# Performance work log

Hardware: AMD Instinct MI355X
Metric: run time of the kernel (lower is better)

The kernel has to match this reference:

```python
import jax, jax.numpy as jnp
import numpy as np

N = 1048576
N_GRID = 256
DX = 1.0 / N_GRID
INV_DX = float(N_GRID)
DT = 2e-5
P_VOL = (DX * 0.5) ** 2
P_RHO = 1.0
P_MASS = P_VOL * P_RHO
E_MOD = 1000.0
NU = 0.2
MU_0 = E_MOD / (2.0 * (1.0 + NU))
LAM_0 = E_MOD * NU / ((1.0 + NU) * (1.0 - 2.0 * NU))
GRAVITY = 50.0


def setup_inputs() -> dict:
    key = jax.random.key(0)
    k = jax.random.split(key, 5)
    x = 0.1 + 0.8 * jax.random.uniform(k[0], (N, 2), dtype=jnp.float32)
    v = 0.1 * jax.random.normal(k[1], (N, 2), dtype=jnp.float32)
    C = 0.5 * jax.random.normal(k[2], (N, 2, 2), dtype=jnp.float32)
    F = jnp.eye(2, dtype=jnp.float32)[None] + 0.1 * jax.random.normal(k[3], (N, 2, 2), dtype=jnp.float32)
    material = jax.random.randint(k[4], (N,), 0, 3, dtype=jnp.int32)
    Jp = jnp.ones((N,), dtype=jnp.float32)
    return {"x": x, "v": v, "C": C, "F": F, "material": material, "Jp": Jp}


def reference(x, v, C, F, material, Jp):
    dt, inv_dx, dx = DT, INV_DX, DX
    base = jnp.floor(x * inv_dx - 0.5).astype(jnp.int32)          # [N,2]
    fx = x * inv_dx - base.astype(x.dtype)                        # [N,2]
    # quadratic B-spline weights, stacked over the 3 taps -> [3,N,2]
    w = jnp.stack([0.5 * (1.5 - fx) ** 2,
                   0.75 - (fx - 1.0) ** 2,
                   0.5 * (fx - 0.5) ** 2], axis=0)

    # deformation gradient update
    F = F + dt * jnp.einsum('nij,njk->nik', C, F)

    h = jnp.exp(10.0 * (1.0 - Jp))
    h = jnp.where(material == 1, 0.3, h)
    mu = jnp.where(material == 0, 0.0, MU_0 * h)
    lam = LAM_0 * h

    # per-particle 2x2 SVD (original pads to 3x3 and slices back)
    U, sig, Vh = jnp.linalg.svd(F)

    # snow plasticity: clamp singular values, track Jp
    clamped = jnp.clip(sig, 1.0 - 2.5e-2, 1.0 + 4.5e-3)
    is_snow = material == 2
    Jp = jnp.where(is_snow, Jp * jnp.prod(sig / clamped, axis=-1), Jp)
    sig = jnp.where(is_snow[:, None], clamped, sig)

    J = jnp.prod(sig, axis=-1)
    eye2 = jnp.eye(2, dtype=x.dtype)
    F_fluid = eye2[None] * jnp.sqrt(J)[:, None, None]             # J^(1/n_dim), n_dim=2
    F_snow = jnp.einsum('nij,nj,njk->nik', U, sig, Vh)
    F = jnp.where((material == 0)[:, None, None], F_fluid,
                  jnp.where(is_snow[:, None, None], F_snow, F))

    R = jnp.einsum('nij,njk->nik', U, Vh)
    stress = (2.0 * mu[:, None, None] * jnp.einsum('nij,nkj->nik', F - R, F)
              + eye2[None] * (lam * J * (J - 1.0))[:, None, None])
    stress = (-dt * P_VOL * 4.0 * inv_dx ** 2) * stress
    affine = stress + P_MASS * C                                   # [N,2,2]

    # ---- P2G scatter over the 3x3 stencil (vectorized over 9 taps) ----
    offs = jnp.array([[i, j] for i in range(3) for j in range(3)], dtype=jnp.int32)  # [9,2]
    weight = w[offs[:, 0], :, 0] * w[offs[:, 1], :, 1]             # [9,N]
    target = base[None, :, :] + offs[:, None, :]                   # [9,N,2]
    idx = target[..., 0] * N_GRID + target[..., 1]                 # [9,N]
    flat_idx = idx.reshape(-1)
    NG2 = N_GRID * N_GRID

    v_add = P_MASS * v - jnp.einsum('nij,nj->ni', affine, x)       # [N,2]
    grid_v = jax.ops.segment_sum((weight[..., None] * v_add[None]).reshape(-1, 2),
                                 flat_idx, num_segments=NG2).reshape(N_GRID, N_GRID, 2)
    grid_affine = jax.ops.segment_sum((weight[..., None, None] * affine[None]).reshape(-1, 4),
                                      flat_idx, num_segments=NG2).reshape(N_GRID, N_GRID, 2, 2)
    grid_m = jax.ops.segment_sum((weight * P_MASS).reshape(-1),
                                 flat_idx, num_segments=NG2).reshape(N_GRID, N_GRID)

    grid_x = jnp.stack(jnp.meshgrid(jnp.arange(N_GRID), jnp.arange(N_GRID), indexing='ij'),
                       axis=-1).astype(x.dtype) * dx               # [G,G,2]
    grid_v = grid_v + jnp.einsum('abij,abj->abi', grid_affine, grid_x)

    # grid ops: momentum -> velocity, gravity, boundary clamps
    m = grid_m[..., None]
    grid_v = jnp.where(m > 0, grid_v / jnp.maximum(m, 1e-12), grid_v)
    grid_v = grid_v.at[:, :, 1].add(-dt * GRAVITY)
    grid_v = grid_v.at[:3, :, 0].max(0.0)
    grid_v = grid_v.at[-2:, :, 0].min(0.0)
    grid_v = grid_v.at[:, :3, 1].max(0.0)
    grid_v = grid_v.at[:, -2:, 1].min(0.0)

    # ---- G2P gather ----
    gvf = grid_v.reshape(NG2, 2)
    g_v = gvf[idx]                                                 # [9,N,2]
    new_v = jnp.sum(weight[..., None] * g_v, axis=0)               # [N,2]
    pos = target.astype(x.dtype) * dx                              # [9,N,2]
    new_C = jnp.sum(weight[..., None, None] * g_v[..., :, None] * pos[..., None, :], axis=0)
    new_C = (new_C - new_v[..., None] * x[:, None, :]) * (4.0 * inv_dx ** 2)

    x = x + dt * new_v
    return (x, new_v, new_C, F, material, Jp)
```

## Files before the change

### kernel.cpp

```cpp
#include <hip/hip_runtime.h>
#include <hip/hip_fp16.h>

#define NG 256
#define NG2 (NG*NG)
#define NREP 8

constexpr float DX      = 1.0f / 256.0f;
constexpr float INV_DX  = 256.0f;
constexpr float DT      = 2e-5f;
constexpr float P_VOL   = (1.0f/512.0f) * (1.0f/512.0f);
constexpr float P_MASS  = P_VOL;
constexpr float MU_0    = 1000.0f / (2.0f * 1.2f);
constexpr float LAM_0   = 1000.0f * 0.2f / (1.2f * 0.6f);
constexpr float GRAV    = 50.0f;
constexpr float KA      = -DT * 4.0f * INV_DX * INV_DX;
constexpr float MINMS   = 1e-12f / P_MASS;

__device__ __forceinline__ int bin_of(float px, float py) {
    int bx = (int)floorf(px * INV_DX - 0.5f);
    int by = (int)floorf(py * INV_DX - 0.5f);
    bx = min(max(bx, 0), NG - 1);
    by = min(max(by, 0), NG - 1);
    return (bx << 8) | by;
}

__device__ __forceinline__ float bw(float t) {
    float at = fabsf(t);
    float a  = fmaxf(1.5f - at, 0.0f);
    float w1 = 0.75f - t * t;
    float w2 = 0.5f * a * a;
    return (at < 0.5f) ? w1 : w2;
}

__device__ __forceinline__ unsigned pack_h2(float a, float b) {
    union { __half2 h; unsigned u; } cv;
    cv.h = __floats2half2_rn(a, b);
    return cv.u;
}
__device__ __forceinline__ float2 unpack_h2(unsigned u) {
    union { __half2 h; unsigned u; } cv;
    cv.u = u;
    return __half22float2(cv.h);
}


__global__ __launch_bounds__(256) void binrank_kernel(
    const float* __restrict__ x, int* __restrict__ counts8,
    unsigned char* __restrict__ rank, int n)
{
    int i = blockIdx.x * blockDim.x + threadIdx.x;
    if (i >= n) return;
    float2 p = ((const float2*)x)[i];
    int b = bin_of(p.x, p.y);
    int rep = (i >> 8) & (NREP - 1);
    rank[i] = (unsigned char)atomicAdd(&counts8[rep * NG2 + b], 1);
}

__global__ __launch_bounds__(256) void scan1_kernel(
    const int* __restrict__ counts8, uint2* __restrict__ offs8,
    int* __restrict__ starts, int* __restrict__ bsum)
{
    __shared__ int tmp[256];
    int t = threadIdx.x, blk = blockIdx.x;
    int b = blk * 256 + t;

    int c0 = counts8[0*NG2 + b], c1 = counts8[1*NG2 + b];
    int c2 = counts8[2*NG2 + b], c3 = counts8[3*NG2 + b];
    int c4 = counts8[4*NG2 + b], c5 = counts8[5*NG2 + b];
    int c6 = counts8[6*NG2 + b], c7 = counts8[7*NG2 + b];
    int o1 = c0, o2 = o1+c1, o3 = o2+c2, o4 = o3+c3;
    int o5 = o4+c4, o6 = o5+c5, o7 = o6+c6;
    int total = o7 + c7;
    uint2 packed;
    packed.x = (unsigned)(o1 << 8) | ((unsigned)o2 << 16) | ((unsigned)o3 << 24);
    packed.y = (unsigned)o4 | ((unsigned)o5 << 8) | ((unsigned)o6 << 16) | ((unsigned)o7 << 24);
    offs8[b] = packed;

    tmp[t] = total;
    __syncthreads();
    #pragma unroll
    for (int off = 1; off < 256; off <<= 1) {
        int add = (t >= off) ? tmp[t - off] : 0;
        __syncthreads();
        tmp[t] += add;
        __syncthreads();
    }
    starts[b] = tmp[t] - total;
    if (t == 255) bsum[blk] = tmp[255];
}

__global__ __launch_bounds__(256) void scan2_kernel(int* __restrict__ bsum)
{
    __shared__ int tmp[256];
    int t = threadIdx.x;
    int v = bsum[t];
    tmp[t] = v;
    __syncthreads();
    #pragma unroll
    for (int off = 1; off < 256; off <<= 1) {
        int add = (t >= off) ? tmp[t - off] : 0;
        __syncthreads();
        tmp[t] += add;
        __syncthreads();
    }
    bsum[t] = tmp[t] - v;
}

__global__ __launch_bounds__(256) void scan3_kernel(
    int* __restrict__ starts, const int* __restrict__ bsum, int n)
{
    int i = blockIdx.x * blockDim.x + threadIdx.x;
    if (i < NG2) starts[i] += bsum[i >> 8];
    if (i == 0) starts[NG2] = n;
}


__global__ __launch_bounds__(256) void compute_scatter_kernel(
    const float* __restrict__ x, const float* __restrict__ v,
    const float* __restrict__ C, const float* __restrict__ F,
    const int* __restrict__ mat, const float* __restrict__ Jp,
    const int* __restrict__ starts, const uint2* __restrict__ offs8,
    const unsigned char* __restrict__ rank,
    uint4* __restrict__ srec,
    float4* __restrict__ F_out4, float* __restrict__ mat_out, float* __restrict__ Jp_out,
    int n)
{
    int i = blockIdx.x * blockDim.x + threadIdx.x;
    if (i >= n) return;

    float2 xp = ((const float2*)x)[i];
    float px = xp.x, py = xp.y;

    int bin = bin_of(px, py);
    int rep = (i >> 8) & (NREP - 1);
    uint2 o8 = offs8[bin];
    int sb = starts[bin];
    int rk = (int)rank[i];

    float2 vp = ((const float2*)v)[i];
    float4 Cp = ((const float4*)C)[i];
    float4 Fp = ((const float4*)F)[i];
    int    m  = mat[i];
    float  jp = Jp[i];

    float C00 = Cp.x, C01 = Cp.y, C10 = Cp.z, C11 = Cp.w;
    float a = Fp.x, b = Fp.y, c = Fp.z, d = Fp.w;

    float na = a + DT*(C00*a + C01*c);
    float nb = b + DT*(C00*b + C01*d);
    float nc = c + DT*(C10*a + C11*c);
    float nd = d + DT*(C10*b + C11*d);
    a = na; b = nb; c = nc; d = nd;

    float h = expf(10.0f * (1.0f - jp));
    if (m == 1) h = 0.3f;
    float mu  = (m == 0) ? 0.0f : MU_0 * h;
    float lam = LAM_0 * h;

    float S00 = a*a + c*c, S01 = a*b + c*d, S11 = b*b + d*d;
    float mh = 0.5f*(S00 + S11), dh = 0.5f*(S00 - S11);
    float delta = sqrtf(dh*dh + S01*S01);
    float sig1 = sqrtf(fmaxf(mh + delta, 0.0f));
    float sig2 = sqrtf(fmaxf(mh - delta, 0.0f));
    float e0, e1;
    if (dh >= 0.0f) { e0 = delta + dh; e1 = S01; }
    else            { e0 = S01;        e1 = delta - dh; }
    float elen = sqrtf(e0*e0 + e1*e1);
    float vc, vs;
    if (elen > 1e-30f) { float il = 1.0f/elen; vc = e0*il; vs = e1*il; }
    else               { vc = 1.0f; vs = 0.0f; }
    float inv1 = 1.0f / fmaxf(sig1, 1e-30f);
    float inv2 = 1.0f / fmaxf(sig2, 1e-30f);
    float u1x = ( a*vc + b*vs) * inv1, u1y = ( c*vc + d*vs) * inv1;
    float u2x = (-a*vs + b*vc) * inv2, u2y = (-c*vs + d*vc) * inv2;

    if (m == 2) {
        float c1 = fminf(fmaxf(sig1, 1.0f - 2.5e-2f), 1.0f + 4.5e-3f);
        float c2 = fminf(fmaxf(sig2, 1.0f - 2.5e-2f), 1.0f + 4.5e-3f);
        jp = jp * (sig1 / c1) * (sig2 / c2);
        sig1 = c1; sig2 = c2;
    }
    float J = sig1 * sig2;

    if (m == 0) {
        float s = sqrtf(J);
        a = s; b = 0.0f; c = 0.0f; d = s;
    } else if (m == 2) {
        a = sig1*u1x*vc - sig2*u2x*vs;
        b = sig1*u1x*vs + sig2*u2x*vc;
        c = sig1*u1y*vc - sig2*u2y*vs;
        d = sig1*u1y*vs + sig2*u2y*vc;
    }
    float R00 = u1x*vc - u2x*vs, R01 = u1x*vs + u2x*vc;
    float R10 = u1y*vc - u2y*vs, R11 = u1y*vs + u2y*vc;

    float k2mu = 2.0f * mu;
    float fr00 = a - R00, fr01 = b - R01, fr10 = c - R10, fr11 = d - R11;
    float ljj  = lam * J * (J - 1.0f);
    float st00 = k2mu*(fr00*a + fr01*b) + ljj;
    float st01 = k2mu*(fr00*c + fr01*d);
    float st10 = k2mu*(fr10*a + fr11*b);
    float st11 = k2mu*(fr10*c + fr11*d) + ljj;

    float A00 = KA*st00 + C00;
    float A01 = KA*st01 + C01;
    float A10 = KA*st10 + C10;
    float A11 = KA*st11 + C11;

    float bxf = floorf(px * INV_DX - 0.5f), byf = floorf(py * INV_DX - 0.5f);
    float fracx = px * INV_DX - bxf - 0.5f;
    float fracy = py * INV_DX - byf - 0.5f;
    float bppx = vp.x - DX * (A00*fracx + A01*fracy);
    float bppy = vp.y - DX * (A10*fracx + A11*fracy);

    unsigned qx = (unsigned)fminf(fracx * 65536.0f, 65535.0f);
    unsigned qy = (unsigned)fminf(fracy * 65536.0f, 65535.0f);

    unsigned offv = (rep < 4 ? (o8.x >> (8*rep)) : (o8.y >> (8*(rep-4)))) & 255u;
    int sidx = sb + (int)offv + rk;

    uint4 rec;
    rec.x = qx | (qy << 16);
    rec.y = pack_h2(bppx, bppy);
    rec.z = pack_h2(A00, A01);
    rec.w = pack_h2(A10, A11);
    srec[sidx] = rec;

    F_out4[i]  = make_float4(a, b, c, d);
    mat_out[i] = (float)m;
    Jp_out[i]  = jp;
}

__global__ __launch_bounds__(256) void gather_grid_kernel(
    const uint4* __restrict__ srec, const int* __restrict__ starts,
    float2* __restrict__ gv)
{
    int bid  = blockIdx.x;
    int swz  = (bid & 7) * (4096 / 8) + (bid >> 3);
    int gtid  = swz * 256 + threadIdx.x;
    int cell  = gtid >> 4;
    int slice = gtid & 15;
    int gi = cell >> 8, gj = cell & (NG - 1);

    float msum = 0.0f, mvx = 0.0f, mvy = 0.0f;

    int b0[4], b1[4], b2[4];
    #pragma unroll
    for (int c = 0; c < 4; ++c) {
        int col = gj - 2 + c;
        int cc = col < 0 ? 0 : col;
        int bi;
        bi = gi - 2; b0[c] = (bi >= 0) ? starts[(bi << 8) + cc] : 0;
        bi = gi - 1; b1[c] = (bi >= 0) ? starts[(bi << 8) + cc] : 0;
        bi = gi;     b2[c] = starts[(bi << 8) + cc];
    }

    #pragma unroll
    for (int t3 = 0; t3 < 3; ++t3) {
        int s, e, m1, m2;
        if (t3 == 0)      { s = b0[0]; m1 = b0[1]; m2 = b0[2]; e = b0[3]; }
        else if (t3 == 1) { s = b1[0]; m1 = b1[1]; m2 = b1[2]; e = b1[3]; }
        else              { s = b2[0]; m1 = b2[1]; m2 = b2[2]; e = b2[3]; }
        float basex = (float)(t3 - 2);
        float dgx   = -(basex + 0.5f) * DX;

        for (int k = s + slice; k < e; k += 16) {
            uint4 r = srec[k];
            int cc = (k >= m1) + (k >= m2);
            float fx = (float)(r.x & 0xffffu) * (1.0f/65536.0f);
            float fy = (float)(r.x >> 16)     * (1.0f/65536.0f);
            float basey = (float)cc - 2.0f;
            float dgy   = -(basey + 0.5f) * DX;
            float w = bw(basex + 0.5f + fx) * bw(basey + 0.5f + fy);
            float2 bb = unpack_h2(r.y);
            float2 a0 = unpack_h2(r.z);
            float2 a1 = unpack_h2(r.w);
            msum += w;
            mvx  += w * (bb.x + a0.x * dgx + a0.y * dgy);
            mvy  += w * (bb.y + a1.x * dgx + a1.y * dgy);
        }
    }

    #pragma unroll
    for (int off = 1; off < 16; off <<= 1) {
        msum += __shfl_xor(msum, off);
        mvx  += __shfl_xor(mvx,  off);
        mvy  += __shfl_xor(mvy,  off);
    }

    if (slice == 0) {
        float vx = mvx, vy = mvy;
        if (msum > 0.0f) {
            float im = 1.0f / fmaxf(msum, MINMS);
            vx *= im; vy *= im;
        }
        vy -= DT * GRAV;
        if (gi < 3)      vx = fmaxf(vx, 0.0f);
        if (gi >= NG-2)  vx = fminf(vx, 0.0f);
        if (gj < 3)      vy = fmaxf(vy, 0.0f);
        if (gj >= NG-2)  vy = fminf(vy, 0.0f);
        gv[cell] = make_float2(vx, vy);
    }
}

__global__ __launch_bounds__(256) void g2p_kernel(
    const float* __restrict__ x, const float2* __restrict__ gv,
    float* __restrict__ x_out, float* __restrict__ v_out, float* __restrict__ C_out,
    int n)
{
    int i = blockIdx.x * blockDim.x + threadIdx.x;
    if (i >= n) return;

    float2 xp = ((const float2*)x)[i];
    float px = xp.x, py = xp.y;
    float bxf = floorf(px * INV_DX - 0.5f), byf = floorf(py * INV_DX - 0.5f);
    float fx = px * INV_DX - bxf, fy = py * INV_DX - byf;
    float wxs[3] = { 0.5f*(1.5f-fx)*(1.5f-fx), 0.75f-(fx-1.0f)*(fx-1.0f), 0.5f*(fx-0.5f)*(fx-0.5f) };
    float wys[3] = { 0.5f*(1.5f-fy)*(1.5f-fy), 0.75f-(fy-1.0f)*(fy-1.0f), 0.5f*(fy-0.5f)*(fy-0.5f) };
    int bix = (int)bxf, biy = (int)byf;

    float nvx = 0.0f, nvy = 0.0f;
    float c00 = 0.0f, c01 = 0.0f, c10 = 0.0f, c11 = 0.0f;
    #pragma unroll
    for (int ii = 0; ii < 3; ++ii) {
        float posx = (bxf + (float)ii) * DX;
        int rowbase = (bix + ii) * NG + biy;
        #pragma unroll
        for (int jj = 0; jj < 3; ++jj) {
            float w = wxs[ii] * wys[jj];
            float posy = (byf + (float)jj) * DX;
            float2 g = gv[rowbase + jj];
            nvx += w * g.x; nvy += w * g.y;
            c00 += w * g.x * posx; c01 += w * g.x * posy;
            c10 += w * g.y * posx; c11 += w * g.y * posy;
        }
    }
    const float K = 4.0f * INV_DX * INV_DX;
    c00 = (c00 - nvx * px) * K; c01 = (c01 - nvx * py) * K;
    c10 = (c10 - nvy * px) * K; c11 = (c11 - nvy * py) * K;

    ((float2*)x_out)[i] = make_float2(px + DT * nvx, py + DT * nvy);
    ((float2*)v_out)[i] = make_float2(nvx, nvy);
    ((float4*)C_out)[i] = make_float4(c00, c01, c10, c11);
}

extern "C" void kernel_launch(void* const* d_in, const int* in_sizes, int n_in,
                              void* d_out, int out_size, void* d_ws, size_t ws_size,
                              hipStream_t stream) {
    const float* x   = (const float*)d_in[0];
    const float* v   = (const float*)d_in[1];
    const float* C   = (const float*)d_in[2];
    const float* F   = (const float*)d_in[3];
    const int*   mat = (const int*)d_in[4];
    const float* Jp  = (const float*)d_in[5];

    int n = in_sizes[0] / 2;

    float* out     = (float*)d_out;
    float* x_out   = out;
    float* v_out   = out + (size_t)2*n;
    float* C_out   = out + (size_t)4*n;
    float* F_out   = out + (size_t)8*n;
    float* mat_out = out + (size_t)12*n;
    float* Jp_out  = out + (size_t)13*n;

    uint4* srec = (uint4*)out;

    int blocks = (n + 255) / 256;

    char* ws = (char*)d_ws;
    size_t off = 0;
    int*   counts8 = (int*)(ws + off);  off += (size_t)NG2 * NREP * 4;
    int*   starts  = (int*)(ws + off);  off += (size_t)(NG2 + 1) * 4;
    uint2* offs8   = (uint2*)(ws + off); off += (size_t)NG2 * 8;
    int*   bsum    = (int*)(ws + off);  off += 256 * 4;
    unsigned char* rank = (unsigned char*)(ws + off); off += (size_t)n;
    off = (off + 63) & ~(size_t)63;
    float2* gv     = (float2*)(ws + off); off += (size_t)NG2 * 8;

    hipMemsetAsync(counts8, 0, (size_t)NG2 * NREP * 4, stream);
    binrank_kernel<<<blocks, 256, 0, stream>>>(x, counts8, rank, n);
    scan1_kernel<<<NG2/256, 256, 0, stream>>>(counts8, offs8, starts, bsum);
    scan2_kernel<<<1, 256, 0, stream>>>(bsum);
    scan3_kernel<<<NG2/256, 256, 0, stream>>>(starts, bsum, n);
    compute_scatter_kernel<<<blocks, 256, 0, stream>>>(x, v, C, F, mat, Jp,
                                                       starts, offs8, rank, srec,
                                                       (float4*)F_out, mat_out, Jp_out, n);
    gather_grid_kernel<<<(NG2*16)/256, 256, 0, stream>>>(srec, starts, gv);
    g2p_kernel<<<blocks, 256, 0, stream>>>(x, gv, x_out, v_out, C_out, n);
}
```

Before: 128.3 us.

## Fuse binning atomics into compute pass and scatter precomputed records in mover kernel

Moves the per-bin atomic rank counting into the particle compute kernel, which now writes packed records and bin/rep/rank metadata to a workspace buffer. A new mover kernel then places each record at its sorted position after the prefix scan. This removes the separate binning pass over positions and takes the heavy math off the scan's critical path. In exchange it adds a full extra write and read of record-sized intermediate data.

```diff
diff --git a/kernel.cpp b/kernel.cpp
--- a/kernel.cpp
+++ b/kernel.cpp
@@ -44,84 +44,12 @@
 }
 
 
-__global__ __launch_bounds__(256) void binrank_kernel(
-    const float* __restrict__ x, int* __restrict__ counts8,
-    unsigned char* __restrict__ rank, int n)
-{
-    int i = blockIdx.x * blockDim.x + threadIdx.x;
-    if (i >= n) return;
-    float2 p = ((const float2*)x)[i];
-    int b = bin_of(p.x, p.y);
-    int rep = (i >> 8) & (NREP - 1);
-    rank[i] = (unsigned char)atomicAdd(&counts8[rep * NG2 + b], 1);
-}
-
-__global__ __launch_bounds__(256) void scan1_kernel(
-    const int* __restrict__ counts8, uint2* __restrict__ offs8,
-    int* __restrict__ starts, int* __restrict__ bsum)
-{
-    __shared__ int tmp[256];
-    int t = threadIdx.x, blk = blockIdx.x;
-    int b = blk * 256 + t;
-
-    int c0 = counts8[0*NG2 + b], c1 = counts8[1*NG2 + b];
-    int c2 = counts8[2*NG2 + b], c3 = counts8[3*NG2 + b];
-    int c4 = counts8[4*NG2 + b], c5 = counts8[5*NG2 + b];
-    int c6 = counts8[6*NG2 + b], c7 = counts8[7*NG2 + b];
-    int o1 = c0, o2 = o1+c1, o3 = o2+c2, o4 = o3+c3;
-    int o5 = o4+c4, o6 = o5+c5, o7 = o6+c6;
-    int total = o7 + c7;
-    uint2 packed;
-    packed.x = (unsigned)(o1 << 8) | ((unsigned)o2 << 16) | ((unsigned)o3 << 24);
-    packed.y = (unsigned)o4 | ((unsigned)o5 << 8) | ((unsigned)o6 << 16) | ((unsigned)o7 << 24);
-    offs8[b] = packed;
-
-    tmp[t] = total;
-    __syncthreads();
-    #pragma unroll
-    for (int off = 1; off < 256; off <<= 1) {
-        int add = (t >= off) ? tmp[t - off] : 0;
-        __syncthreads();
-        tmp[t] += add;
-        __syncthreads();
-    }
-    starts[b] = tmp[t] - total;
-    if (t == 255) bsum[blk] = tmp[255];
-}
-
-__global__ __launch_bounds__(256) void scan2_kernel(int* __restrict__ bsum)
-{
-    __shared__ int tmp[256];
-    int t = threadIdx.x;
-    int v = bsum[t];
-    tmp[t] = v;
-    __syncthreads();
-    #pragma unroll
-    for (int off = 1; off < 256; off <<= 1) {
-        int add = (t >= off) ? tmp[t - off] : 0;
-        __syncthreads();
-        tmp[t] += add;
-        __syncthreads();
-    }
-    bsum[t] = tmp[t] - v;
-}
-
-__global__ __launch_bounds__(256) void scan3_kernel(
-    int* __restrict__ starts, const int* __restrict__ bsum, int n)
-{
-    int i = blockIdx.x * blockDim.x + threadIdx.x;
-    if (i < NG2) starts[i] += bsum[i >> 8];
-    if (i == 0) starts[NG2] = n;
-}
-
-
-__global__ __launch_bounds__(256) void compute_scatter_kernel(
+__global__ __launch_bounds__(256) void compute_count_kernel(
     const float* __restrict__ x, const float* __restrict__ v,
     const float* __restrict__ C, const float* __restrict__ F,
     const int* __restrict__ mat, const float* __restrict__ Jp,
-    const int* __restrict__ starts, const uint2* __restrict__ offs8,
-    const unsigned char* __restrict__ rank,
-    uint4* __restrict__ srec,
+    int* __restrict__ counts8,
+    uint4* __restrict__ payload, unsigned* __restrict__ meta,
     float4* __restrict__ F_out4, float* __restrict__ mat_out, float* __restrict__ Jp_out,
     int n)
 {
@@ -133,9 +61,7 @@
 
     int bin = bin_of(px, py);
     int rep = (i >> 8) & (NREP - 1);
-    uint2 o8 = offs8[bin];
-    int sb = starts[bin];
-    int rk = (int)rank[i];
+    int rk  = atomicAdd(&counts8[rep * NG2 + bin], 1);
 
     float2 vp = ((const float2*)v)[i];
     float4 Cp = ((const float4*)C)[i];
@@ -216,19 +142,94 @@
     unsigned qx = (unsigned)fminf(fracx * 65536.0f, 65535.0f);
     unsigned qy = (unsigned)fminf(fracy * 65536.0f, 65535.0f);
 
-    unsigned offv = (rep < 4 ? (o8.x >> (8*rep)) : (o8.y >> (8*(rep-4)))) & 255u;
-    int sidx = sb + (int)offv + rk;
-
     uint4 rec;
     rec.x = qx | (qy << 16);
     rec.y = pack_h2(bppx, bppy);
     rec.z = pack_h2(A00, A01);
     rec.w = pack_h2(A10, A11);
-    srec[sidx] = rec;
+    payload[i] = rec;
+    meta[i] = (unsigned)bin | ((unsigned)rep << 16) | ((unsigned)rk << 19);
 
     F_out4[i]  = make_float4(a, b, c, d);
     mat_out[i] = (float)m;
     Jp_out[i]  = jp;
+}
+
+
+__global__ __launch_bounds__(256) void scan1_kernel(
+    const int* __restrict__ counts8, uint2* __restrict__ offs8,
+    int* __restrict__ starts, int* __restrict__ bsum)
+{
+    __shared__ int tmp[256];
+    int t = threadIdx.x, blk = blockIdx.x;
+    int b = blk * 256 + t;
+
+    int c0 = counts8[0*NG2 + b], c1 = counts8[1*NG2 + b];
+    int c2 = counts8[2*NG2 + b], c3 = counts8[3*NG2 + b];
+    int c4 = counts8[4*NG2 + b], c5 = counts8[5*NG2 + b];
+    int c6 = counts8[6*NG2 + b], c7 = counts8[7*NG2 + b];
+    int o1 = c0, o2 = o1+c1, o3 = o2+c2, o4 = o3+c3;
+    int o5 = o4+c4, o6 = o5+c5, o7 = o6+c6;
+    int total = o7 + c7;
+    uint2 packed;
+    packed.x = (unsigned)(o1 << 8) | ((unsigned)o2 << 16) | ((unsigned)o3 << 24);
+    packed.y = (unsigned)o4 | ((unsigned)o5 << 8) | ((unsigned)o6 << 16) | ((unsigned)o7 << 24);
+    offs8[b] = packed;
+
+    tmp[t] = total;
+    __syncthreads();
+    #pragma unroll
+    for (int off = 1; off < 256; off <<= 1) {
+        int add = (t >= off) ? tmp[t - off] : 0;
+        __syncthreads();
+        tmp[t] += add;
+        __syncthreads();
+    }
+    starts[b] = tmp[t] - total;
+    if (t == 255) bsum[blk] = tmp[255];
+}
+
+__global__ __launch_bounds__(256) void scan2_kernel(int* __restrict__ bsum)
+{
+    __shared__ int tmp[256];
+    int t = threadIdx.x;
+    int v = bsum[t];
+    tmp[t] = v;
+    __syncthreads();
+    #pragma unroll
+    for (int off = 1; off < 256; off <<= 1) {
+        int add = (t >= off) ? tmp[t - off] : 0;
+        __syncthreads();
+        tmp[t] += add;
+        __syncthreads();
+    }
+    bsum[t] = tmp[t] - v;
+}
+
+__global__ __launch_bounds__(256) void scan3_kernel(
+    int* __restrict__ starts, const int* __restrict__ bsum, int n)
+{
+    int i = blockIdx.x * blockDim.x + threadIdx.x;
+    if (i < NG2) starts[i] += bsum[i >> 8];
+    if (i == 0) starts[NG2] = n;
+}
+
+
+__global__ __launch_bounds__(256) void mover_kernel(
+    const uint4* __restrict__ payload, const unsigned* __restrict__ meta,
+    const int* __restrict__ starts, const uint2* __restrict__ offs8,
+    uint4* __restrict__ srec, int n)
+{
+    int i = blockIdx.x * blockDim.x + threadIdx.x;
+    if (i >= n) return;
+    unsigned mt = meta[i];
+    int bin = (int)(mt & 0xffffu);
+    int rep = (int)((mt >> 16) & 7u);
+    int rk  = (int)(mt >> 19);
+    uint2 o8 = offs8[bin];
+    int sb = starts[bin];
+    unsigned offv = (rep < 4 ? (o8.x >> (8*rep)) : (o8.y >> (8*(rep-4)))) & 255u;
+    srec[sb + (int)offv + rk] = payload[i];
 }
 
 __global__ __launch_bounds__(256) void gather_grid_kernel(
@@ -374,18 +375,20 @@
     int*   starts  = (int*)(ws + off);  off += (size_t)(NG2 + 1) * 4;
     uint2* offs8   = (uint2*)(ws + off); off += (size_t)NG2 * 8;
     int*   bsum    = (int*)(ws + off);  off += 256 * 4;
-    unsigned char* rank = (unsigned char*)(ws + off); off += (size_t)n;
+    off = (off + 63) & ~(size_t)63;
+    uint4* payload = (uint4*)(ws + off); off += (size_t)n * 16;
+    unsigned* meta = (unsigned*)(ws + off); off += (size_t)n * 4;
     off = (off + 63) & ~(size_t)63;
     float2* gv     = (float2*)(ws + off); off += (size_t)NG2 * 8;
 
     hipMemsetAsync(counts8, 0, (size_t)NG2 * NREP * 4, stream);
-    binrank_kernel<<<blocks, 256, 0, stream>>>(x, counts8, rank, n);
+    compute_count_kernel<<<blocks, 256, 0, stream>>>(x, v, C, F, mat, Jp,
+                                                     counts8, payload, meta,
+                                                     (float4*)F_out, mat_out, Jp_out, n);
     scan1_kernel<<<NG2/256, 256, 0, stream>>>(counts8, offs8, starts, bsum);
     scan2_kernel<<<1, 256, 0, stream>>>(bsum);
     scan3_kernel<<<NG2/256, 256, 0, stream>>>(starts, bsum, n);
-    compute_scatter_kernel<<<blocks, 256, 0, stream>>>(x, v, C, F, mat, Jp,
-                                                       starts, offs8, rank, srec,
-                                                       (float4*)F_out, mat_out, Jp_out, n);
+    mover_kernel<<<blocks, 256, 0, stream>>>(payload, meta, starts, offs8, srec, n);
     gather_grid_kernel<<<(NG2*16)/256, 256, 0, stream>>>(srec, starts, gv);
     g2p_kernel<<<blocks, 256, 0, stream>>>(x, gv, x_out, v_out, C_out, n);
 }
```

New measurement: 127.1 us. No clear change (-0.9%).
